# Performance work log

Measured on AMD Instinct MI355X. Metric: run time of the kernel, lower is better.

Reference implementation:

```python
import jax, jax.numpy as jnp
import numpy as np

IN_FEATURES = 8192
OUT_FEATURES = 8192
CODESZ = 8
CB_SIZE = 256


def fwht(x):
    """Orthonormal Walsh-Hadamard transform along last dim (power of 2).
    Equivalent to x @ H / sqrt(n) with Sylvester Hadamard H (symmetric),
    so it implements both matmul_hadU and matmul_hadUt for K=1."""
    b, n = x.shape
    h = 2
    while h <= n:
        x = x.reshape(b, n // h, h)
        half = h // 2
        a, c = x[..., :half], x[..., half:]
        x = jnp.concatenate([a + c, a - c], axis=-1)
        h *= 2
    return x.reshape(b, n) * jnp.asarray(1.0 / np.sqrt(n), x.dtype)


def setup_inputs() -> dict:
    key = jax.random.key(0)
    ks = jax.random.split(key, 8)
    inp = jax.random.normal(ks[0], (32, 4, IN_FEATURES), dtype=jnp.float16)
    Qidxs = jax.random.randint(ks[1], (OUT_FEATURES, IN_FEATURES // CODESZ), 0, CB_SIZE, dtype=jnp.int32)
    codebook_table = jax.random.normal(ks[2], (CB_SIZE, CODESZ), dtype=jnp.float32).astype(jnp.float16)
    # positive per-column rescale (scaleWH buffer)
    scaleWH = (0.5 + jax.random.uniform(ks[3], (IN_FEATURES,), dtype=jnp.float32)).astype(jnp.float16)
    # random sign vectors SU/SV (stored as int8 +-1 in torch; used as fp16 multipliers)
    SU = jnp.where(jax.random.uniform(ks[4], (IN_FEATURES,)) < 0.5, -1.0, 1.0).astype(jnp.float16)
    SV = jnp.where(jax.random.uniform(ks[5], (OUT_FEATURES,)) < 0.5, -1.0, 1.0).astype(jnp.float16)
    Wscale = jnp.asarray(0.02, dtype=jnp.float16)
    bias = (0.01 * jax.random.normal(ks[6], (OUT_FEATURES,), dtype=jnp.float32)).astype(jnp.float16)
    return {"input": inp, "Qidxs": Qidxs, "codebook_table": codebook_table,
            "scaleWH": scaleWH, "SU": SU, "SV": SV, "Wscale": Wscale, "bias": bias}


def reference(input, Qidxs, codebook_table, scaleWH, SU, SV, Wscale, bias):
    x = input.reshape(-1, IN_FEATURES).astype(jnp.float16)
    # rescale_WH + SU sign flip, fused elementwise
    x = (x / scaleWH) * SU
    # matmul_hadUt_cuda (in_features is a power of 2 -> pure orthonormal WHT)
    x = fwht(x)
    # codebook dequant + GEMM: W_hat[o, i] = codebook[Qidxs[o, i//8], i%8] * Wscale
    W_hat = codebook_table[Qidxs].reshape(OUT_FEATURES, IN_FEATURES) * Wscale  # [out, in] fp16
    out = x @ W_hat.T  # [tokens, out]
    # matmul_hadU_cuda on output side (power of 2, no truncation needed)
    out = fwht(out)
    out = out * SV + bias
    return out.reshape(input.shape[:-1] + (OUT_FEATURES,))
```

## Files before the change

### kernel.cpp

```cpp
#include <hip/hip_runtime.h>
#include <hip/hip_bf16.h>

#define IN_F 8192
#define OUT_F 8192
#define NROWS 128
#define CB 256
#define NSL 8
#define KSLICE (IN_F / NSL)
#define NTB 128
#define QC (IN_F / 8)

using bf8    = __attribute__((ext_vector_type(8))) short;
using f32x16 = __attribute__((ext_vector_type(16))) float;

typedef const __attribute__((address_space(1))) void* as1cv;
typedef __attribute__((address_space(3))) void* as3v;

__device__ inline float bf2f(unsigned int u) {
    union { unsigned int i; float f; } v; v.i = u << 16; return v.f;
}
__device__ inline unsigned short f2bf(float f) {
    __hip_bfloat16 h = __float2bfloat16(f);
    return *reinterpret_cast<unsigned short*>(&h);
}
__device__ inline void unpack8(uint4 v, float* f) {
    f[0] = bf2f(v.x & 0xffffu); f[1] = bf2f(v.x >> 16);
    f[2] = bf2f(v.y & 0xffffu); f[3] = bf2f(v.y >> 16);
    f[4] = bf2f(v.z & 0xffffu); f[5] = bf2f(v.z >> 16);
    f[6] = bf2f(v.w & 0xffffu); f[7] = bf2f(v.w >> 16);
}

#define FWHT_SCALE 0.011048543456039806f

#define FWHT16(v)                                                         \
    _Pragma("unroll")                                                     \
    for (int hb = 0; hb < 4; ++hb) {                                      \
        const int hh = 1 << hb;                                           \
        _Pragma("unroll")                                                 \
        for (int j = 0; j < 16; ++j)                                      \
            if (!(j & hh)) {                                              \
                float a_ = v[j], b_ = v[j | hh];                          \
                v[j] = a_ + b_; v[j | hh] = a_ - b_;                      \
            }                                                             \
    }

__device__ inline void fwht4096(float* v, float* lds, int t) {
    FWHT16(v)
#pragma unroll
    for (int e = 0; e < 16; ++e) lds[e * 260 + t] = v[e];
    __syncthreads();
    {
        const int base = (t & 15) * 260 + (t >> 4) * 16;
#pragma unroll
        for (int q = 0; q < 4; ++q) {
            float4 f = *reinterpret_cast<const float4*>(&lds[base + q * 4]);
            v[q * 4 + 0] = f.x; v[q * 4 + 1] = f.y;
            v[q * 4 + 2] = f.z; v[q * 4 + 3] = f.w;
        }
    }
    FWHT16(v)
    __syncthreads();
    {
        const int e = t & 15, ub = t >> 4;
#pragma unroll
        for (int i = 0; i < 16; ++i) lds[e * 260 + i * 16 + ub] = v[i];
    }
    __syncthreads();
    {
        const int e = t & 15, i = t >> 4;
#pragma unroll
        for (int ub = 0; ub < 16; ++ub) v[ub] = lds[e * 260 + i * 16 + ub];
    }
    FWHT16(v)
    __syncthreads();
    {
        const int e = t & 15, i = t >> 4;
#pragma unroll
        for (int ub = 0; ub < 16; ++ub) lds[ub * 260 + i * 16 + e] = v[ub];
    }
    __syncthreads();
    {
        const int base = (t >> 4) * 260 + (t & 15) * 16;
#pragma unroll
        for (int q = 0; q < 4; ++q) {
            float4 f = *reinterpret_cast<const float4*>(&lds[base + q * 4]);
            v[q * 4 + 0] = f.x; v[q * 4 + 1] = f.y;
            v[q * 4 + 2] = f.z; v[q * 4 + 3] = f.w;
        }
    }
}

__global__ __launch_bounds__(256) void k_pre5(const float* __restrict__ in,
                                              const float* __restrict__ scaleWH,
                                              const float* __restrict__ SU,
                                              unsigned short* __restrict__ xt) {
    __shared__ float lds[4160];
    const int r = blockIdx.x, h = blockIdx.y, t = threadIdx.x;
    float v[16];
    const float4* xp = reinterpret_cast<const float4*>(in + (size_t)r * IN_F);
    const float4* sp = reinterpret_cast<const float4*>(scaleWH);
    const float4* up = reinterpret_cast<const float4*>(SU);
#pragma unroll
    for (int q = 0; q < 4; ++q) {
        float4 xl = xp[t * 4 + q],        sl = sp[t * 4 + q],        ul = up[t * 4 + q];
        float4 xh = xp[1024 + t * 4 + q], sh = sp[1024 + t * 4 + q], uh = up[1024 + t * 4 + q];
        float lo0 = xl.x / sl.x * ul.x, hi0 = xh.x / sh.x * uh.x;
        float lo1 = xl.y / sl.y * ul.y, hi1 = xh.y / sh.y * uh.y;
        float lo2 = xl.z / sl.z * ul.z, hi2 = xh.z / sh.z * uh.z;
        float lo3 = xl.w / sl.w * ul.w, hi3 = xh.w / sh.w * uh.w;
        v[q * 4 + 0] = h ? lo0 - hi0 : lo0 + hi0;
        v[q * 4 + 1] = h ? lo1 - hi1 : lo1 + hi1;
        v[q * 4 + 2] = h ? lo2 - hi2 : lo2 + hi2;
        v[q * 4 + 3] = h ? lo3 - hi3 : lo3 + hi3;
    }
    fwht4096(v, lds, t);
    const int k0 = h * 4096 + (t >> 4) * 256 + (t & 15) * 16;
    const size_t base = ((size_t)(r >> 5) * 512 + (k0 >> 4)) * 512 + (size_t)(r & 31) * 8;
#pragma unroll
    for (int half = 0; half < 2; ++half) {
        unsigned int w[4];
#pragma unroll
        for (int p = 0; p < 4; ++p) {
            unsigned int lo = f2bf(v[half * 8 + 2 * p]     * FWHT_SCALE);
            unsigned int hi = f2bf(v[half * 8 + 2 * p + 1] * FWHT_SCALE);
            w[p] = lo | (hi << 16);
        }
        *reinterpret_cast<uint4*>(xt + base + half * 256) = make_uint4(w[0], w[1], w[2], w[3]);
    }
}

__global__ __launch_bounds__(256, 2) void k_gemm12(
        const unsigned short* __restrict__ xt,
        const int* __restrict__ Qidxs,
        const float* __restrict__ cb,
        const float* __restrict__ wscale,
        unsigned short* __restrict__ pout) {
    __shared__ __align__(16) unsigned short cbl[CB][8];
    __shared__ __align__(16) int Qlds[2][8192];
    const int tid = threadIdx.x;
    const int wave = tid >> 6, lane = tid & 63;
    const int ln31 = lane & 31, lh = lane >> 5;
    const int n0 = blockIdx.x * NTB;
    const int ks0 = blockIdx.y * KSLICE;
    const int ksb2 = ks0 >> 4;
    const int c0 = ks0 >> 3;

    auto stageQ = [&](int h) {
#pragma unroll
        for (int j = 0; j < 8; ++j) {
            const int row = j * 16 + wave * 4 + (lane >> 4);
            const int cgs = (lane & 15) ^ (row & 7);
            const int* g = Qidxs + (size_t)(n0 + row) * QC + c0 + h * 64 + cgs * 4;
            as3v l = (as3v)(&Qlds[h][(j * 16 + wave * 4) * 64]);
            __builtin_amdgcn_global_load_lds((as1cv)(const void*)g, l, 16, 0, 0);
        }
    };

    stageQ(0);
    const float wsc = wscale[0];
    for (int e = tid; e < CB * 8; e += 256) cbl[e >> 3][e & 7] = f2bf(cb[e] * wsc);

    f32x16 acc[4];
#pragma unroll
    for (int mt = 0; mt < 4; ++mt)
#pragma unroll
        for (int r2 = 0; r2 < 16; ++r2) acc[mt][r2] = 0.f;

    const unsigned short* xw0 = xt + ((size_t)(0 * 512) + ksb2) * 512 + lane * 8;
    const unsigned short* xw1 = xt + ((size_t)(1 * 512) + ksb2) * 512 + lane * 8;
    const unsigned short* xw2 = xt + ((size_t)(2 * 512) + ksb2) * 512 + lane * 8;
    const unsigned short* xw3 = xt + ((size_t)(3 * 512) + ksb2) * 512 + lane * 8;

    const int qrow = wave * 32 + ln31;
    const int qs7 = qrow & 7;
    const int qb = qrow * 64;

#define QR(H, ITL) (Qlds[H][qb + (((((ITL) * 2 + lh) >> 2) ^ qs7) << 2) + (((ITL) * 2 + lh) & 3)])
#define GA(Q) (*(const bf8*)&cbl[(Q)][0])
#define LA(D, IT) {                                                           \
        D##0 = *(const bf8*)(xw0 + (size_t)(IT) * 512);                       \
        D##1 = *(const bf8*)(xw1 + (size_t)(IT) * 512);                       \
        D##2 = *(const bf8*)(xw2 + (size_t)(IT) * 512);                       \
        D##3 = *(const bf8*)(xw3 + (size_t)(IT) * 512); }
#define MFMA4(A_, B_) {                                                       \
        acc[0] = __builtin_amdgcn_mfma_f32_32x32x16_bf16(A_##0, B_, acc[0], 0, 0, 0); \
        acc[1] = __builtin_amdgcn_mfma_f32_32x32x16_bf16(A_##1, B_, acc[1], 0, 0, 0); \
        acc[2] = __builtin_amdgcn_mfma_f32_32x32x16_bf16(A_##2, B_, acc[2], 0, 0, 0); \
        acc[3] = __builtin_amdgcn_mfma_f32_32x32x16_bf16(A_##3, B_, acc[3], 0, 0, 0); }

#define CHUNK(H) {                                                            \
        int qE = QR(H, 0), qO = QR(H, 1);                                     \
        bf8 aE0, aE1, aE2, aE3, aO0, aO1, aO2, aO3;                           \
        LA(aE, (H) * 32 + 0) LA(aO, (H) * 32 + 1)                             \
        bf8 bE = GA(qE), bO;                                                  \
        _Pragma("unroll")                                                     \
        for (int i2 = 0; i2 < 16; ++i2) {                                     \
            const int itl = i2 * 2;                                           \
            if (i2 < 15) qE = QR(H, itl + 2);                                 \
            bO = GA(qO);                                                      \
            MFMA4(aE, bE)                                                     \
            if (i2 < 15) LA(aE, (H) * 32 + itl + 2)                           \
            if (i2 < 15) qO = QR(H, itl + 3);                                 \
            if (i2 < 15) bE = GA(qE);                                         \
            MFMA4(aO, bO)                                                     \
            if (i2 < 15) LA(aO, (H) * 32 + itl + 3)                           \
        } }

    __syncthreads();
    stageQ(1);
    CHUNK(0)
    __syncthreads();
    CHUNK(1)
#undef CHUNK
#undef MFMA4
#undef LA
#undef GA
#undef QR

    unsigned short* ps = pout + (size_t)blockIdx.y * (NROWS * OUT_F);
    const int col = n0 + wave * 32 + ln31;
#pragma unroll
    for (int mt = 0; mt < 4; ++mt)
#pragma unroll
        for (int r2 = 0; r2 < 16; ++r2) {
            const int row = mt * 32 + (r2 & 3) + 8 * (r2 >> 2) + 4 * lh;
            ps[(size_t)row * OUT_F + col] = f2bf(acc[mt][r2]);
        }
}

__global__ __launch_bounds__(256) void k_post4(const unsigned short* __restrict__ pin,
                                               const float* __restrict__ SV,
                                               const float* __restrict__ bias,
                                               float* __restrict__ out) {
    __shared__ float lds[4160];
    const int r = blockIdx.x, h = blockIdx.y, t = threadIdx.x;
    float lo[16], hi[16], v[16];
#pragma unroll
    for (int j = 0; j < 16; ++j) { lo[j] = 0.f; hi[j] = 0.f; }
#pragma unroll 1
    for (int sl = 0; sl < NSL; ++sl) {
        const uint4* pl = reinterpret_cast<const uint4*>(
            pin + (size_t)sl * NROWS * OUT_F + (size_t)r * OUT_F + t * 16);
        const uint4* ph = reinterpret_cast<const uint4*>(
            pin + (size_t)sl * NROWS * OUT_F + (size_t)r * OUT_F + 4096 + t * 16);
        float a[8], b[8];
        unpack8(pl[0], a); unpack8(pl[1], b);
#pragma unroll
        for (int j = 0; j < 8; ++j) { lo[j] += a[j]; lo[8 + j] += b[j]; }
        unpack8(ph[0], a); unpack8(ph[1], b);
#pragma unroll
        for (int j = 0; j < 8; ++j) { hi[j] += a[j]; hi[8 + j] += b[j]; }
    }
#pragma unroll
    for (int j = 0; j < 16; ++j) v[j] = h ? lo[j] - hi[j] : lo[j] + hi[j];
    fwht4096(v, lds, t);
    const int cb4 = (h * 4096 + (t >> 4) * 256 + (t & 15) * 16) >> 2;
    const float4* svp = reinterpret_cast<const float4*>(SV);
    const float4* bip = reinterpret_cast<const float4*>(bias);
    float4* op = reinterpret_cast<float4*>(out + (size_t)r * OUT_F);
#pragma unroll
    for (int q = 0; q < 4; ++q) {
        float4 sv = svp[cb4 + q], bi = bip[cb4 + q], o;
        o.x = v[q * 4 + 0] * FWHT_SCALE * sv.x + bi.x;
        o.y = v[q * 4 + 1] * FWHT_SCALE * sv.y + bi.y;
        o.z = v[q * 4 + 2] * FWHT_SCALE * sv.z + bi.z;
        o.w = v[q * 4 + 3] * FWHT_SCALE * sv.w + bi.w;
        op[cb4 + q] = o;
    }
}

extern "C" void kernel_launch(void* const* d_in, const int* in_sizes, int n_in,
                              void* d_out, int out_size, void* d_ws, size_t ws_size,
                              hipStream_t stream) {
    const float* in      = (const float*)d_in[0];
    const int*   Qidxs   = (const int*)d_in[1];
    const float* cb      = (const float*)d_in[2];
    const float* scaleWH = (const float*)d_in[3];
    const float* SU      = (const float*)d_in[4];
    const float* SV      = (const float*)d_in[5];
    const float* wscale  = (const float*)d_in[6];
    const float* bias    = (const float*)d_in[7];
    float* out = (float*)d_out;

    unsigned short* xt    = (unsigned short*)d_ws;
    unsigned short* parts = (unsigned short*)((char*)d_ws
                            + (size_t)NROWS * IN_F * 2);

    k_pre5<<<dim3(NROWS, 2), 256, 0, stream>>>(in, scaleWH, SU, xt);
    k_gemm12<<<dim3(OUT_F / NTB, NSL), 256, 0, stream>>>(xt, Qidxs, cb, wscale, parts);
    k_post4<<<dim3(NROWS, 2), 256, 0, stream>>>(parts, SV, bias, out);
}
```

Measured before the change: 54.55 us.

## Split GEMM block K range across two wave groups with doubled partial slices

The GEMM block grows from 256 to 512 threads. The two halves of the block's K slice are processed concurrently by separate wave groups instead of sequentially in two chunks. Both Q index halves are staged up front, which removes the mid-loop barrier. Each wave group writes its own partial buffer, so the post kernel now reduces 16 partial slices instead of 8. This roughly doubles partial-sum write and read traffic and needs twice the workspace, in exchange for more waves per CU to hide latency.

Result: slower. 139.8 us (+156.3%).

```diff
diff --git a/kernel.cpp b/kernel.cpp
--- a/kernel.cpp
+++ b/kernel.cpp
@@ -6,6 +6,7 @@
 #define NROWS 128
 #define CB 256
 #define NSL 8
+#define NSLT 16
 #define KSLICE (IN_F / NSL)
 #define NTB 128
 #define QC (IN_F / 8)
@@ -129,7 +130,7 @@
     }
 }
 
-__global__ __launch_bounds__(256, 2) void k_gemm12(
+__global__ __launch_bounds__(512, 4) void k_gemm13(
         const unsigned short* __restrict__ xt,
         const int* __restrict__ Qidxs,
         const float* __restrict__ cb,
@@ -139,6 +140,7 @@
     __shared__ __align__(16) int Qlds[2][8192];
     const int tid = threadIdx.x;
     const int wave = tid >> 6, lane = tid & 63;
+    const int nblk = wave & 3, kh = wave >> 2;
     const int ln31 = lane & 31, lh = lane >> 5;
     const int n0 = blockIdx.x * NTB;
     const int ks0 = blockIdx.y * KSLICE;
@@ -147,18 +149,19 @@
 
     auto stageQ = [&](int h) {
 #pragma unroll
-        for (int j = 0; j < 8; ++j) {
-            const int row = j * 16 + wave * 4 + (lane >> 4);
+        for (int j = 0; j < 4; ++j) {
+            const int row = j * 32 + wave * 4 + (lane >> 4);
             const int cgs = (lane & 15) ^ (row & 7);
             const int* g = Qidxs + (size_t)(n0 + row) * QC + c0 + h * 64 + cgs * 4;
-            as3v l = (as3v)(&Qlds[h][(j * 16 + wave * 4) * 64]);
+            as3v l = (as3v)(&Qlds[h][(j * 32 + wave * 4) * 64]);
             __builtin_amdgcn_global_load_lds((as1cv)(const void*)g, l, 16, 0, 0);
         }
     };
 
     stageQ(0);
+    stageQ(1);
     const float wsc = wscale[0];
-    for (int e = tid; e < CB * 8; e += 256) cbl[e >> 3][e & 7] = f2bf(cb[e] * wsc);
+    for (int e = tid; e < CB * 8; e += 512) cbl[e >> 3][e & 7] = f2bf(cb[e] * wsc);
 
     f32x16 acc[4];
 #pragma unroll
@@ -166,16 +169,16 @@
 #pragma unroll
         for (int r2 = 0; r2 < 16; ++r2) acc[mt][r2] = 0.f;
 
-    const unsigned short* xw0 = xt + ((size_t)(0 * 512) + ksb2) * 512 + lane * 8;
-    const unsigned short* xw1 = xt + ((size_t)(1 * 512) + ksb2) * 512 + lane * 8;
-    const unsigned short* xw2 = xt + ((size_t)(2 * 512) + ksb2) * 512 + lane * 8;
-    const unsigned short* xw3 = xt + ((size_t)(3 * 512) + ksb2) * 512 + lane * 8;
-
-    const int qrow = wave * 32 + ln31;
+    const unsigned short* xw0 = xt + ((size_t)(0 * 512) + ksb2 + kh * 32) * 512 + lane * 8;
+    const unsigned short* xw1 = xt + ((size_t)(1 * 512) + ksb2 + kh * 32) * 512 + lane * 8;
+    const unsigned short* xw2 = xt + ((size_t)(2 * 512) + ksb2 + kh * 32) * 512 + lane * 8;
+    const unsigned short* xw3 = xt + ((size_t)(3 * 512) + ksb2 + kh * 32) * 512 + lane * 8;
+
+    const int qrow = nblk * 32 + ln31;
     const int qs7 = qrow & 7;
     const int qb = qrow * 64;
 
-#define QR(H, ITL) (Qlds[H][qb + (((((ITL) * 2 + lh) >> 2) ^ qs7) << 2) + (((ITL) * 2 + lh) & 3)])
+#define QR(ITL) (Qlds[kh][qb + (((((ITL) * 2 + lh) >> 2) ^ qs7) << 2) + (((ITL) * 2 + lh) & 3)])
 #define GA(Q) (*(const bf8*)&cbl[(Q)][0])
 #define LA(D, IT) {                                                           \
         D##0 = *(const bf8*)(xw0 + (size_t)(IT) * 512);                       \
@@ -188,37 +191,33 @@
         acc[2] = __builtin_amdgcn_mfma_f32_32x32x16_bf16(A_##2, B_, acc[2], 0, 0, 0); \
         acc[3] = __builtin_amdgcn_mfma_f32_32x32x16_bf16(A_##3, B_, acc[3], 0, 0, 0); }
 
-#define CHUNK(H) {                                                            \
-        int qE = QR(H, 0), qO = QR(H, 1);                                     \
-        bf8 aE0, aE1, aE2, aE3, aO0, aO1, aO2, aO3;                           \
-        LA(aE, (H) * 32 + 0) LA(aO, (H) * 32 + 1)                             \
-        bf8 bE = GA(qE), bO;                                                  \
-        _Pragma("unroll")                                                     \
-        for (int i2 = 0; i2 < 16; ++i2) {                                     \
-            const int itl = i2 * 2;                                           \
-            if (i2 < 15) qE = QR(H, itl + 2);                                 \
-            bO = GA(qO);                                                      \
-            MFMA4(aE, bE)                                                     \
-            if (i2 < 15) LA(aE, (H) * 32 + itl + 2)                           \
-            if (i2 < 15) qO = QR(H, itl + 3);                                 \
-            if (i2 < 15) bE = GA(qE);                                         \
-            MFMA4(aO, bO)                                                     \
-            if (i2 < 15) LA(aO, (H) * 32 + itl + 3)                           \
-        } }
-
-    __syncthreads();
-    stageQ(1);
-    CHUNK(0)
-    __syncthreads();
-    CHUNK(1)
-#undef CHUNK
+    __syncthreads();
+
+    {
+        int qE = QR(0), qO = QR(1);
+        bf8 aE0, aE1, aE2, aE3, aO0, aO1, aO2, aO3;
+        LA(aE, 0) LA(aO, 1)
+        bf8 bE = GA(qE), bO;
+#pragma unroll
+        for (int i2 = 0; i2 < 16; ++i2) {
+            const int itl = i2 * 2;
+            if (i2 < 15) qE = QR(itl + 2);
+            bO = GA(qO);
+            MFMA4(aE, bE)
+            if (i2 < 15) LA(aE, itl + 2)
+            if (i2 < 15) qO = QR(itl + 3);
+            if (i2 < 15) bE = GA(qE);
+            MFMA4(aO, bO)
+            if (i2 < 15) LA(aO, itl + 3)
+        }
+    }
 #undef MFMA4
 #undef LA
 #undef GA
 #undef QR
 
-    unsigned short* ps = pout + (size_t)blockIdx.y * (NROWS * OUT_F);
-    const int col = n0 + wave * 32 + ln31;
+    unsigned short* ps = pout + (size_t)(blockIdx.y * 2 + kh) * (NROWS * OUT_F);
+    const int col = n0 + nblk * 32 + ln31;
 #pragma unroll
     for (int mt = 0; mt < 4; ++mt)
 #pragma unroll
@@ -228,7 +227,7 @@
         }
 }
 
-__global__ __launch_bounds__(256) void k_post4(const unsigned short* __restrict__ pin,
+__global__ __launch_bounds__(256) void k_post5(const unsigned short* __restrict__ pin,
                                                const float* __restrict__ SV,
                                                const float* __restrict__ bias,
                                                float* __restrict__ out) {
@@ -238,7 +237,7 @@
 #pragma unroll
     for (int j = 0; j < 16; ++j) { lo[j] = 0.f; hi[j] = 0.f; }
 #pragma unroll 1
-    for (int sl = 0; sl < NSL; ++sl) {
+    for (int sl = 0; sl < NSLT; ++sl) {
         const uint4* pl = reinterpret_cast<const uint4*>(
             pin + (size_t)sl * NROWS * OUT_F + (size_t)r * OUT_F + t * 16);
         const uint4* ph = reinterpret_cast<const uint4*>(
@@ -287,6 +286,6 @@
                             + (size_t)NROWS * IN_F * 2);
 
     k_pre5<<<dim3(NROWS, 2), 256, 0, stream>>>(in, scaleWH, SU, xt);
-    k_gemm12<<<dim3(OUT_F / NTB, NSL), 256, 0, stream>>>(xt, Qidxs, cb, wscale, parts);
-    k_post4<<<dim3(NROWS, 2), 256, 0, stream>>>(parts, SV, bias, out);
-}
+    k_gemm13<<<dim3(OUT_F / NTB, NSL), 512, 0, stream>>>(xt, Qidxs, cb, wscale, parts);
+    k_post5<<<dim3(NROWS, 2), 256, 0, stream>>>(parts, SV, bias, out);
+}
```
